# Kernel optimization log

Measured on AMD Instinct MI355X. Metric: run time of the kernel, lower is better.

Reference implementation:

```python
import jax, jax.numpy as jnp
import numpy as np

B, S, D_MODEL, H = 4, 2048, 1024, 16
D_K = D_MODEL // H


def setup_inputs() -> dict:
    key = jax.random.key(0)
    kx, kq, kk, kv, ko = jax.random.split(key, 5)
    scale = 1.0 / np.sqrt(D_MODEL)
    return {
        "x": jax.random.normal(kx, (B, S, D_MODEL), dtype=jnp.float32),
        "W_q": jax.random.normal(kq, (D_MODEL, D_MODEL), dtype=jnp.float32) * scale,
        "W_k": jax.random.normal(kk, (D_MODEL, D_MODEL), dtype=jnp.float32) * scale,
        "W_v": jax.random.normal(kv, (D_MODEL, D_MODEL), dtype=jnp.float32) * scale,
        "W_out": jax.random.normal(ko, (D_MODEL, D_MODEL), dtype=jnp.float32) * scale,
    }


def reference(x, W_q, W_k, W_v, W_out):
    # nn.Linear(bias=False): y = x @ W.T; weights stored as (out, in).
    Bx, Sx, D = x.shape
    q = (x @ W_q.T).reshape(Bx, Sx, H, D_K).transpose(0, 2, 1, 3)  # (B,H,S,d_k)
    k = (x @ W_k.T).reshape(Bx, Sx, H, D_K).transpose(0, 2, 1, 3)
    v = (x @ W_v.T).reshape(Bx, Sx, H, D_K).transpose(0, 2, 1, 3)
    scores = jnp.einsum("bhsd,bhtd->bhst", q, k) / jnp.sqrt(jnp.float32(D_K))
    attn = jax.nn.softmax(scores, axis=-1)
    out = jnp.einsum("bhst,bhtd->bhsd", attn, v)  # (B,H,S,d_k)
    out = out.transpose(0, 2, 1, 3).reshape(Bx, Sx, D)  # combine heads
    return out @ W_out.T
```

## Files before the change

kernel.cpp:

```cpp
#include <hip/hip_runtime.h>

#define BATCH 4
#define SEQ 2048
#define DM 1024
#define NH 16
#define DK 64

typedef unsigned short u16;
typedef unsigned int u32;
typedef __attribute__((ext_vector_type(8))) short bfrag;
typedef __attribute__((ext_vector_type(4))) short bfrag4;
typedef __attribute__((ext_vector_type(4))) float ffrag;

__device__ inline u16 f2bf(float f) {
  union { float f; u32 u; } v; v.f = f;
  u32 u = v.u;
  return (u16)((u + 0x7FFFu + ((u >> 16) & 1u)) >> 16);
}
__device__ inline float bf2f(u16 u) {
  union { u32 u; float f; } v; v.u = ((u32)u) << 16;
  return v.f;
}
__device__ inline ffrag MFMA(bfrag a, bfrag b, ffrag c) {
  return __builtin_amdgcn_mfma_f32_16x16x32_bf16(a, b, c, 0, 0, 0);
}
#if defined(__has_builtin)
#if __has_builtin(__builtin_amdgcn_mfma_f32_16x16x16bf16_1k)
#define HAVE_MFMA16 1
#endif
#endif
#if HAVE_MFMA16
__device__ inline ffrag MFMA16(bfrag4 a, bfrag4 b, ffrag c) {
  return __builtin_amdgcn_mfma_f32_16x16x16bf16_1k(a, b, c, 0, 0, 0);
}
#else
__device__ inline ffrag MFMA16(bfrag4 a, bfrag4 b, ffrag c) { return c; }
#endif

__device__ __forceinline__ void g2l16(const u16* g, u16* l) {
  __builtin_amdgcn_global_load_lds(
      (const __attribute__((address_space(1))) u16*)g,
      (__attribute__((address_space(3))) u16*)l, 16, 0, 0);
}

__global__ __launch_bounds__(256) void cvt_all(
    const float* __restrict__ x,
    const float* __restrict__ a, const float* __restrict__ b,
    const float* __restrict__ c, const float* __restrict__ d,
    u16* __restrict__ ox,
    u16* __restrict__ oa, u16* __restrict__ ob,
    u16* __restrict__ oc, u16* __restrict__ od) {
  int blk = blockIdx.x;
  const float* in;
  u16* out;
  int i;
  if (blk < 8192) {
    in = x; out = ox; i = blk * 256 + threadIdx.x;
  } else {
    int wb = blk - 8192;
    int which = wb >> 10;
    in = which == 0 ? a : which == 1 ? b : which == 2 ? c : d;
    out = which == 0 ? oa : which == 1 ? ob : which == 2 ? oc : od;
    i = (wb & 1023) * 256 + threadIdx.x;
  }
  float4 v = ((const float4*)in)[i];
  union { u16 u[4]; uint2 dd; } o;
  o.u[0] = f2bf(v.x); o.u[1] = f2bf(v.y); o.u[2] = f2bf(v.z); o.u[3] = f2bf(v.w);
  ((uint2*)out)[i] = o.dd;
}

__global__ __launch_bounds__(256) void gemm_qkv(
    const u16* __restrict__ xb,
    const u16* __restrict__ Wq, const u16* __restrict__ Wk,
    const u16* __restrict__ Wv,
    u16* __restrict__ Qb, u16* __restrict__ Ksw, u16* __restrict__ Vsw) {
  const int z = blockIdx.z;
  const u16* Bm = z == 0 ? Wq : z == 1 ? Wk : Wv;

  const int K = DM;
  const int bm = blockIdx.y * 128, bn = blockIdx.x * 128;
  __shared__ __align__(16) u16 As[128 * 32];
  __shared__ __align__(16) u16 Bs[128 * 32];
  const int tid = threadIdx.x;
  const int lane = tid & 63;
  const int w = tid >> 6;
  const int wr = w >> 1, wc = w & 1;
  const int l15 = lane & 15, quad = lane >> 4;
  const int srow = tid >> 2, scol = (tid & 3) * 8;

  ffrag acc[4][4] = {};

  for (int k0 = 0; k0 < K; k0 += 32) {
    __syncthreads();
    g2l16(&xb[(size_t)(bm + srow) * K + k0 + scol], &As[tid * 8]);
    g2l16(&xb[(size_t)(bm + 64 + srow) * K + k0 + scol], &As[(tid + 256) * 8]);
    g2l16(&Bm[(size_t)(bn + srow) * K + k0 + scol], &Bs[tid * 8]);
    g2l16(&Bm[(size_t)(bn + 64 + srow) * K + k0 + scol], &Bs[(tid + 256) * 8]);
    __syncthreads();
    bfrag af[4], bf[4];
    if (z < 2) {
#pragma unroll
      for (int i = 0; i < 4; i++)
        af[i] = *(const bfrag*)(&As[(wr * 64 + i * 16 + l15) * 32 + quad * 8]);
#pragma unroll
      for (int j = 0; j < 4; j++)
        bf[j] = *(const bfrag*)(&Bs[(wc * 64 + j * 16 + l15) * 32 + quad * 8]);
    } else {
#pragma unroll
      for (int i = 0; i < 4; i++)
        af[i] = *(const bfrag*)(&Bs[(wr * 64 + i * 16 + l15) * 32 + quad * 8]);
#pragma unroll
      for (int j = 0; j < 4; j++)
        bf[j] = *(const bfrag*)(&As[(wc * 64 + j * 16 + l15) * 32 + quad * 8]);
    }
#pragma unroll
    for (int i = 0; i < 4; i++)
#pragma unroll
      for (int j = 0; j < 4; j++)
        acc[i][j] = MFMA(af[i], bf[j], acc[i][j]);
  }

  if (z == 0) {
#pragma unroll
    for (int i = 0; i < 4; i++)
#pragma unroll
      for (int j = 0; j < 4; j++)
#pragma unroll
        for (int r = 0; r < 4; r++) {
          int m = bm + wr * 64 + i * 16 + quad * 4 + r;
          int n = bn + wc * 64 + j * 16 + l15;
          int b = m >> 11, s = m & 2047;
          int h = n >> 6, d = n & 63;
          Qb[(((size_t)(b * NH + h)) * SEQ + s) * DK + d] = f2bf(acc[i][j][r]);
        }
  } else if (z == 1) {
#pragma unroll
    for (int i = 0; i < 4; i++)
#pragma unroll
      for (int j = 0; j < 4; j++)
#pragma unroll
        for (int r = 0; r < 4; r++) {
          int m = bm + wr * 64 + i * 16 + quad * 4 + r;
          int n = bn + wc * 64 + j * 16 + l15;
          int b = m >> 11, s = m & 2047;
          int h = n >> 6, d = n & 63;
          size_t hb = (size_t)(b * NH + h) * (SEQ * DK);
          size_t off = hb + (size_t)(s >> 6) * 4096 +
              ((((s >> 4) & 3) * 2 + (d >> 5)) * 64 +
               ((d >> 3) & 3) * 16 + (s & 15)) * 8 + (d & 7);
          Ksw[off] = f2bf(acc[i][j][r]);
        }
  } else {
#pragma unroll
    for (int i = 0; i < 4; i++)
#pragma unroll
      for (int j = 0; j < 4; j++)
#pragma unroll
        for (int r = 0; r < 4; r++) {
          int n = bn + wr * 64 + i * 16 + quad * 4 + r;
          int m = bm + wc * 64 + j * 16 + l15;
          int b = m >> 11, s = m & 2047;
          int h = n >> 6, d = n & 63;
          size_t hb = (size_t)(b * NH + h) * (SEQ * DK);
          size_t off = hb + (size_t)(s >> 6) * 4096 +
              ((((d >> 4) * 4 + ((s >> 4) & 3)) * 64 +
                ((s >> 2) & 3) * 16 + (d & 15)) * 4 + (s & 3));
          Vsw[off] = f2bf(acc[i][j][r]);
        }
  }
}

__global__ __launch_bounds__(256) void gemm_out(
    const u16* __restrict__ Ab, const u16* __restrict__ Wo, float* __restrict__ C) {
  const int K = DM, N = DM;
  const int bm = blockIdx.y * 128, bn = blockIdx.x * 128;
  __shared__ __align__(16) u16 As[128 * 32];
  __shared__ __align__(16) u16 Bs[128 * 32];
  const int tid = threadIdx.x;
  const int lane = tid & 63;
  const int w = tid >> 6;
  const int wr = w >> 1, wc = w & 1;
  const int l15 = lane & 15, quad = lane >> 4;
  const int srow = tid >> 2, scol = (tid & 3) * 8;

  ffrag acc[4][4] = {};

  for (int k0 = 0; k0 < K; k0 += 32) {
    __syncthreads();
    g2l16(&Ab[(size_t)(bm + srow) * K + k0 + scol], &As[tid * 8]);
    g2l16(&Ab[(size_t)(bm + 64 + srow) * K + k0 + scol], &As[(tid + 256) * 8]);
    g2l16(&Wo[(size_t)(bn + srow) * K + k0 + scol], &Bs[tid * 8]);
    g2l16(&Wo[(size_t)(bn + 64 + srow) * K + k0 + scol], &Bs[(tid + 256) * 8]);
    __syncthreads();
    bfrag af[4], bf[4];
#pragma unroll
    for (int i = 0; i < 4; i++)
      af[i] = *(const bfrag*)(&As[(wr * 64 + i * 16 + l15) * 32 + quad * 8]);
#pragma unroll
    for (int j = 0; j < 4; j++)
      bf[j] = *(const bfrag*)(&Bs[(wc * 64 + j * 16 + l15) * 32 + quad * 8]);
#pragma unroll
    for (int i = 0; i < 4; i++)
#pragma unroll
      for (int j = 0; j < 4; j++)
        acc[i][j] = MFMA(af[i], bf[j], acc[i][j]);
  }

#pragma unroll
  for (int i = 0; i < 4; i++)
#pragma unroll
    for (int j = 0; j < 4; j++)
#pragma unroll
      for (int r = 0; r < 4; r++) {
        int m = bm + wr * 64 + i * 16 + quad * 4 + r;
        int n = bn + wc * 64 + j * 16 + l15;
        C[(size_t)m * N + n] = acc[i][j][r];
      }
}

__global__ __launch_bounds__(256) void attn(
    const u16* __restrict__ Qb, const u16* __restrict__ Ksw,
    const u16* __restrict__ Vsw, u16* __restrict__ Ab) {
  const int bh = blockIdx.y;
  const int b = bh >> 4, h = bh & 15;
  const int qbase = blockIdx.x * 128;
  const int tid = threadIdx.x;
  const int w = tid >> 6, lane = tid & 63;
  const int l15 = lane & 15, quad = lane >> 4;

  __shared__ __align__(16) u16 Kt[2][4096];
  __shared__ __align__(16) u16 Vt[2][4096];

  const size_t hbase = (size_t)bh * SEQ * DK;

  const float qscale = 0.125f * 1.4426950408889634f;
  bfrag q[2][2];
#pragma unroll
  for (int i = 0; i < 2; i++)
#pragma unroll
    for (int kk = 0; kk < 2; kk++) {
      bfrag t = *(const bfrag*)(&Qb[hbase +
          (size_t)(qbase + w * 32 + i * 16 + l15) * DK + kk * 32 + quad * 8]);
#pragma unroll
      for (int e = 0; e < 8; e++)
        q[i][kk][e] = (short)f2bf(bf2f((u16)t[e]) * qscale);
    }

  ffrag O[4][2] = {};
  float lsum[2] = {0.f, 0.f};

  {
    const u16* ks = &Ksw[hbase];
    const u16* vs = &Vsw[hbase];
    g2l16(&ks[tid * 8], &Kt[0][tid * 8]);
    g2l16(&ks[2048 + tid * 8], &Kt[0][2048 + tid * 8]);
    g2l16(&vs[tid * 8], &Vt[0][tid * 8]);
    g2l16(&vs[2048 + tid * 8], &Vt[0][2048 + tid * 8]);
  }

  for (int t = 0; t < SEQ / 64; t++) {
    const int buf = t & 1;
    __syncthreads();
    if (t + 1 < SEQ / 64) {
      const u16* ks = &Ksw[hbase + (size_t)(t + 1) * 4096];
      const u16* vs = &Vsw[hbase + (size_t)(t + 1) * 4096];
      g2l16(&ks[tid * 8], &Kt[buf ^ 1][tid * 8]);
      g2l16(&ks[2048 + tid * 8], &Kt[buf ^ 1][2048 + tid * 8]);
      g2l16(&vs[tid * 8], &Vt[buf ^ 1][tid * 8]);
      g2l16(&vs[2048 + tid * 8], &Vt[buf ^ 1][2048 + tid * 8]);
    }

    __builtin_amdgcn_s_setprio(1);
    bfrag4 pb[4][2];
#pragma unroll
    for (int j = 0; j < 4; j++) {
      bfrag k0f = *(const bfrag*)(&Kt[buf][((j * 2 + 0) * 64 + lane) * 8]);
      bfrag k1f = *(const bfrag*)(&Kt[buf][((j * 2 + 1) * 64 + lane) * 8]);
#pragma unroll
      for (int i = 0; i < 2; i++) {
        ffrag z = {};
        z = MFMA(k0f, q[i][0], z);
        z = MFMA(k1f, q[i][1], z);
        u32 u[4]; float ts = 0.f;
#pragma unroll
        for (int r = 0; r < 4; r++) {
          float p = __builtin_amdgcn_exp2f(z[r]);
          u[r] = __float_as_uint(p);
          ts += __uint_as_float(u[r] & 0xffff0000u);
        }
        lsum[i] += ts;
        union { u32 d[2]; bfrag4 v; } pk;
        pk.d[0] = (u[1] & 0xffff0000u) | (u[0] >> 16);
        pk.d[1] = (u[3] & 0xffff0000u) | (u[2] >> 16);
        pb[j][i] = pk.v;
      }
    }

#pragma unroll
    for (int j = 0; j < 4; j++)
#pragma unroll
      for (int db = 0; db < 4; db++) {
        bfrag4 vf = *(const bfrag4*)(&Vt[buf][((db * 4 + j) * 64 + lane) * 4]);
        O[db][0] = MFMA16(vf, pb[j][0], O[db][0]);
        O[db][1] = MFMA16(vf, pb[j][1], O[db][1]);
      }
    __builtin_amdgcn_s_setprio(0);
  }

  float rl[2];
#pragma unroll
  for (int i = 0; i < 2; i++) {
    float s = lsum[i];
    s += __shfl_xor(s, 16);
    s += __shfl_xor(s, 32);
    rl[i] = 1.0f / s;
  }

  const size_t obase = ((size_t)b * SEQ) * DM + (size_t)h * DK;
#pragma unroll
  for (int db = 0; db < 4; db++)
#pragma unroll
    for (int i = 0; i < 2; i++) {
      int s = qbase + w * 32 + i * 16 + l15;
      union { u16 u[4]; uint2 d; } o;
#pragma unroll
      for (int r = 0; r < 4; r++) o.u[r] = f2bf(O[db][i][r] * rl[i]);
      *(uint2*)(&Ab[obase + (size_t)s * DM + db * 16 + quad * 4]) = o.d;
    }
}

extern "C" void kernel_launch(void* const* d_in, const int* in_sizes, int n_in,
                              void* d_out, int out_size, void* d_ws, size_t ws_size,
                              hipStream_t stream) {
  const float* x  = (const float*)d_in[0];
  const float* Wq = (const float*)d_in[1];
  const float* Wk = (const float*)d_in[2];
  const float* Wv = (const float*)d_in[3];
  const float* Wo = (const float*)d_in[4];
  float* out = (float*)d_out;

  char* ws = (char*)d_ws;
  u16* xb  = (u16*)(ws + 0);
  u16* Wqb = (u16*)(ws + 16777216);
  u16* Wkb = (u16*)(ws + 18874368);
  u16* Wvb = (u16*)(ws + 20971520);
  u16* Wob = (u16*)(ws + 23068672);
  u16* Qb  = (u16*)(ws + 25165824);
  u16* Ksw = (u16*)(ws + 41943040);
  u16* Vsw = (u16*)(ws + 58720256);
  u16* Ab  = (u16*)(ws + 75497472);
  const size_t NEED = 92274688;
  if (ws_size < NEED) return;

  cvt_all<<<12288, 256, 0, stream>>>(x, Wq, Wk, Wv, Wo, xb, Wqb, Wkb, Wvb, Wob);

  dim3 gqkv(DM / 128, (BATCH * SEQ) / 128, 3);
  gemm_qkv<<<gqkv, 256, 0, stream>>>(xb, Wqb, Wkb, Wvb, Qb, Ksw, Vsw);

  dim3 gat(SEQ / 128, BATCH * NH);
  attn<<<gat, 256, 0, stream>>>(Qb, Ksw, Vsw, Ab);

  dim3 gout(DM / 128, (BATCH * SEQ) / 128);
  gemm_out<<<gout, 256, 0, stream>>>(Ab, Wob, out);
}
```

Baseline: 292.4 us.

## Halve attention query tile per block and compute row sums via MFMA with ones

Each attention block now handles 64 queries instead of 128 (16 per wave), doubling the grid so more blocks are available to fill the CUs, at the cost of loading each K/V tile twice as often. The softmax denominator is now accumulated with an extra MFMA against a vector of bf16 ones instead of scalar adds plus cross-lane shuffles, which moves that work onto the matrix unit. Per-wave register use drops, which may allow higher occupancy, but global and LDS traffic for K/V per query roughly doubles.

```diff
diff --git a/kernel.cpp b/kernel.cpp
--- a/kernel.cpp
+++ b/kernel.cpp
@@ -223,7 +223,7 @@
     const u16* __restrict__ Vsw, u16* __restrict__ Ab) {
   const int bh = blockIdx.y;
   const int b = bh >> 4, h = bh & 15;
-  const int qbase = blockIdx.x * 128;
+  const int qbase = blockIdx.x * 64;
   const int tid = threadIdx.x;
   const int w = tid >> 6, lane = tid & 63;
   const int l15 = lane & 15, quad = lane >> 4;
@@ -234,20 +234,20 @@
   const size_t hbase = (size_t)bh * SEQ * DK;
 
   const float qscale = 0.125f * 1.4426950408889634f;
-  bfrag q[2][2];
-#pragma unroll
-  for (int i = 0; i < 2; i++)
-#pragma unroll
-    for (int kk = 0; kk < 2; kk++) {
-      bfrag t = *(const bfrag*)(&Qb[hbase +
-          (size_t)(qbase + w * 32 + i * 16 + l15) * DK + kk * 32 + quad * 8]);
-#pragma unroll
-      for (int e = 0; e < 8; e++)
-        q[i][kk][e] = (short)f2bf(bf2f((u16)t[e]) * qscale);
-    }
-
-  ffrag O[4][2] = {};
-  float lsum[2] = {0.f, 0.f};
+  bfrag q[2];
+#pragma unroll
+  for (int kk = 0; kk < 2; kk++) {
+    bfrag t = *(const bfrag*)(&Qb[hbase +
+        (size_t)(qbase + w * 16 + l15) * DK + kk * 32 + quad * 8]);
+#pragma unroll
+    for (int e = 0; e < 8; e++)
+      q[kk][e] = (short)f2bf(bf2f((u16)t[e]) * qscale);
+  }
+
+  const bfrag4 ones = {(short)0x3F80, (short)0x3F80, (short)0x3F80, (short)0x3F80};
+
+  ffrag O[4] = {};
+  ffrag Ls = {};
 
   {
     const u16* ks = &Ksw[hbase];
@@ -271,29 +271,23 @@
     }
 
     __builtin_amdgcn_s_setprio(1);
-    bfrag4 pb[4][2];
+    bfrag4 pb[4];
 #pragma unroll
     for (int j = 0; j < 4; j++) {
       bfrag k0f = *(const bfrag*)(&Kt[buf][((j * 2 + 0) * 64 + lane) * 8]);
       bfrag k1f = *(const bfrag*)(&Kt[buf][((j * 2 + 1) * 64 + lane) * 8]);
-#pragma unroll
-      for (int i = 0; i < 2; i++) {
-        ffrag z = {};
-        z = MFMA(k0f, q[i][0], z);
-        z = MFMA(k1f, q[i][1], z);
-        u32 u[4]; float ts = 0.f;
-#pragma unroll
-        for (int r = 0; r < 4; r++) {
-          float p = __builtin_amdgcn_exp2f(z[r]);
-          u[r] = __float_as_uint(p);
-          ts += __uint_as_float(u[r] & 0xffff0000u);
-        }
-        lsum[i] += ts;
-        union { u32 d[2]; bfrag4 v; } pk;
-        pk.d[0] = (u[1] & 0xffff0000u) | (u[0] >> 16);
-        pk.d[1] = (u[3] & 0xffff0000u) | (u[2] >> 16);
-        pb[j][i] = pk.v;
-      }
+      ffrag z = {};
+      z = MFMA(k0f, q[0], z);
+      z = MFMA(k1f, q[1], z);
+      u32 u0 = __float_as_uint(__builtin_amdgcn_exp2f(z[0]));
+      u32 u1 = __float_as_uint(__builtin_amdgcn_exp2f(z[1]));
+      u32 u2 = __float_as_uint(__builtin_amdgcn_exp2f(z[2]));
+      u32 u3 = __float_as_uint(__builtin_amdgcn_exp2f(z[3]));
+      union { u32 d[2]; bfrag4 v; } pk;
+      pk.d[0] = (u1 & 0xffff0000u) | (u0 >> 16);
+      pk.d[1] = (u3 & 0xffff0000u) | (u2 >> 16);
+      pb[j] = pk.v;
+      Ls = MFMA16(ones, pb[j], Ls);
     }
 
 #pragma unroll
@@ -301,32 +295,22 @@
 #pragma unroll
       for (int db = 0; db < 4; db++) {
         bfrag4 vf = *(const bfrag4*)(&Vt[buf][((db * 4 + j) * 64 + lane) * 4]);
-        O[db][0] = MFMA16(vf, pb[j][0], O[db][0]);
-        O[db][1] = MFMA16(vf, pb[j][1], O[db][1]);
+        O[db] = MFMA16(vf, pb[j], O[db]);
       }
     __builtin_amdgcn_s_setprio(0);
   }
 
-  float rl[2];
-#pragma unroll
-  for (int i = 0; i < 2; i++) {
-    float s = lsum[i];
-    s += __shfl_xor(s, 16);
-    s += __shfl_xor(s, 32);
-    rl[i] = 1.0f / s;
-  }
+  const float rl = 1.0f / Ls[0];
 
   const size_t obase = ((size_t)b * SEQ) * DM + (size_t)h * DK;
-#pragma unroll
-  for (int db = 0; db < 4; db++)
-#pragma unroll
-    for (int i = 0; i < 2; i++) {
-      int s = qbase + w * 32 + i * 16 + l15;
-      union { u16 u[4]; uint2 d; } o;
-#pragma unroll
-      for (int r = 0; r < 4; r++) o.u[r] = f2bf(O[db][i][r] * rl[i]);
-      *(uint2*)(&Ab[obase + (size_t)s * DM + db * 16 + quad * 4]) = o.d;
-    }
+  const int s = qbase + w * 16 + l15;
+#pragma unroll
+  for (int db = 0; db < 4; db++) {
+    union { u16 u[4]; uint2 d; } o;
+#pragma unroll
+    for (int r = 0; r < 4; r++) o.u[r] = f2bf(O[db][r] * rl);
+    *(uint2*)(&Ab[obase + (size_t)s * DM + db * 16 + quad * 4]) = o.d;
+  }
 }
 
 extern "C" void kernel_launch(void* const* d_in, const int* in_sizes, int n_in,
@@ -357,7 +341,7 @@
   dim3 gqkv(DM / 128, (BATCH * SEQ) / 128, 3);
   gemm_qkv<<<gqkv, 256, 0, stream>>>(xb, Wqb, Wkb, Wvb, Qb, Ksw, Vsw);
 
-  dim3 gat(SEQ / 128, BATCH * NH);
+  dim3 gat(SEQ / 64, BATCH * NH);
   attn<<<gat, 256, 0, stream>>>(Qb, Ksw, Vsw, Ab);
 
   dim3 gout(DM / 128, (BATCH * SEQ) / 128);
```

Result: slower. 309.2 us (+5.7%).
